# Kernel optimization log

Measured on AMD Instinct MI355X. Metric: run time of the kernel, lower is better.

Reference implementation:

```python
import jax, jax.numpy as jnp
import numpy as np

N, E, F_IN, C, D = 50000, 200000, 384, 384, 16
NEG_SLOPE = 0.2


def setup_inputs() -> dict:
    key = jax.random.key(0)
    ks = jax.random.split(key, 12)
    x = jax.random.normal(ks[0], (N, F_IN), jnp.float32)
    # random edges with no self-loops (PyG GATConv removes self loops before re-adding them)
    src = jax.random.randint(ks[1], (E,), 0, N)
    off = jax.random.randint(ks[2], (E,), 1, N)
    dst = (src + off) % N
    edge_index = jnp.stack([src, dst]).astype(jnp.int32)  # [2, E]
    edge_attr = jax.random.uniform(ks[3], (E, D), jnp.float32)
    # GATConv params (heads=1): lin (no bias), att_src/att_dst/att_edge, lin_edge (no bias), bias
    W_lin = jax.random.normal(ks[4], (F_IN, C), jnp.float32) / np.float32(np.sqrt(F_IN))
    att_src = jax.random.normal(ks[5], (C,), jnp.float32) * 0.1
    att_dst = jax.random.normal(ks[6], (C,), jnp.float32) * 0.1
    W_edge = jax.random.normal(ks[7], (D, C), jnp.float32) / np.float32(np.sqrt(D))
    att_edge = jax.random.normal(ks[8], (C,), jnp.float32) * 0.1
    bias_conv = jnp.zeros((C,), jnp.float32)
    # final Linear(384 -> 1) with bias
    W_out = jax.random.normal(ks[9], (C, 1), jnp.float32) / np.float32(np.sqrt(C))
    b_out = jnp.zeros((1,), jnp.float32)
    return {"x": x, "edge_index": edge_index, "edge_attr": edge_attr,
            "W_lin": W_lin, "att_src": att_src, "att_dst": att_dst,
            "W_edge": W_edge, "att_edge": att_edge, "bias_conv": bias_conv,
            "W_out": W_out, "b_out": b_out}


def _gat_conv(x, edge_index, edge_attr, W_lin, att_src, att_dst, W_edge, att_edge, bias_conv):
    src, dst = edge_index[0], edge_index[1]
    h = x @ W_lin                              # [N, C]
    a_src = h @ att_src                        # [N]
    a_dst = h @ att_dst                        # [N]
    # add self loops; self-loop edge_attr = per-node mean of incoming edge_attr (fill_value='mean')
    deg = jax.ops.segment_sum(jnp.ones((E,), x.dtype), dst, num_segments=N)
    ea_mean = jax.ops.segment_sum(edge_attr, dst, num_segments=N) / jnp.maximum(deg, 1.0)[:, None]
    loop = jnp.arange(N, dtype=src.dtype)
    src_f = jnp.concatenate([src, loop])       # [E+N]
    dst_f = jnp.concatenate([dst, loop])
    ea_f = jnp.concatenate([edge_attr, ea_mean], axis=0)  # [E+N, D]
    a_edge = (ea_f @ W_edge) @ att_edge        # [E+N]
    # per-edge attention logits, segment softmax over destination neighborhoods
    alpha = jax.nn.leaky_relu(a_src[src_f] + a_dst[dst_f] + a_edge, NEG_SLOPE)
    amax = jax.ops.segment_max(alpha, dst_f, num_segments=N)  # every node has a self loop
    ex = jnp.exp(alpha - amax[dst_f])
    denom = jax.ops.segment_sum(ex, dst_f, num_segments=N)
    w = ex / denom[dst_f]                      # [E+N]
    # weighted scatter-aggregate of source messages
    out = jax.ops.segment_sum(h[src_f] * w[:, None], dst_f, num_segments=N)
    return out + bias_conv


def reference(x, edge_index, edge_attr, W_lin, att_src, att_dst, W_edge, att_edge, bias_conv, W_out, b_out):
    h = _gat_conv(x, edge_index, edge_attr, W_lin, att_src, att_dst, W_edge, att_edge, bias_conv)
    return jax.nn.relu(h @ W_out + b_out)      # [N, 1]
```

## Files before the change

kernel.cpp:

```cpp
#include <hip/hip_runtime.h>

#define NEG_SLOPE 0.2f
#define TPB    256
#define NB     256
#define CNT    196
#define EBLK   256
#define PERBLK 32
#define ER     4
#define MAGIC  21913099ULL
#define NODE_BLKS 1568

__global__ __launch_bounds__(TPB) void k_fold(
        const float* __restrict__ Wlin, const float* __restrict__ att_src,
        const float* __restrict__ att_dst, const float* __restrict__ Wedge,
        const float* __restrict__ att_edge, const float* __restrict__ bias_conv,
        const float* __restrict__ Wout, const float* __restrict__ bout,
        float* __restrict__ vs, float* __restrict__ va, float* __restrict__ vb,
        float* __restrict__ we, float* __restrict__ cb) {
    const int gwid = (blockIdx.x * TPB + threadIdx.x) >> 6;
    const int lane = threadIdx.x & 63;
    for (int j = 0; j < 4; ++j) {
        int f = gwid * 4 + j;
        if (f < 384) {
            float a = 0.f, b = 0.f, c = 0.f;
            for (int k = lane; k < 384; k += 64) {
                float w = Wlin[f * 384 + k];
                a += w * Wout[k];
                b += w * att_src[k];
                c += w * att_dst[k];
            }
            for (int off = 32; off > 0; off >>= 1) {
                a += __shfl_down(a, off);
                b += __shfl_down(b, off);
                c += __shfl_down(c, off);
            }
            if (lane == 0) { vs[f] = a; va[f] = b; vb[f] = c; }
        } else if (f < 400) {
            int d = f - 384;
            float a = 0.f;
            for (int k = lane; k < 384; k += 64) a += Wedge[d * 384 + k] * att_edge[k];
            for (int off = 32; off > 0; off >>= 1) a += __shfl_down(a, off);
            if (lane == 0) we[d] = a;
        } else if (f == 400) {
            float a = 0.f;
            for (int k = lane; k < 384; k += 64) a += bias_conv[k] * Wout[k];
            for (int off = 32; off > 0; off >>= 1) a += __shfl_down(a, off);
            if (lane == 0) cb[0] = a + bout[0];
        }
    }
}

__global__ __launch_bounds__(TPB) void k_main(
        const float* __restrict__ x,
        const int* __restrict__ src, const int* __restrict__ dst,
        const float* __restrict__ ea,
        const float* __restrict__ vs, const float* __restrict__ va,
        const float* __restrict__ vb, const float* __restrict__ we,
        float* __restrict__ s, float* __restrict__ asrc, float* __restrict__ adst,
        uint2* __restrict__ rec, unsigned int* __restrict__ cnt,
        int N, int E) {
    __shared__ float weL[16];
    __shared__ int   ldsCnt[NB];
    const int tid = threadIdx.x;
    const int blk = blockIdx.x;

    if (blk < NODE_BLKS) {
        const int ll = tid & 15;
        const int slot = blk * 16 + (tid >> 4);
        const float4* vs4 = (const float4*)vs;
        const float4* va4 = (const float4*)va;
        const float4* vb4 = (const float4*)vb;
        float4 wsr[6], war[6], wbr[6];
#pragma unroll
        for (int j = 0; j < 6; ++j) {
            wsr[j] = vs4[ll + 16 * j];
            war[j] = va4[ll + 16 * j];
            wbr[j] = vb4[ll + 16 * j];
        }
        for (int n = slot; n < N; n += NODE_BLKS * 16) {
            const float4* row = (const float4*)(x + (size_t)n * 384);
            float4 xr[6];
#pragma unroll
            for (int j = 0; j < 6; ++j) xr[j] = row[ll + 16 * j];
            float a = 0.f, b = 0.f, c = 0.f;
#pragma unroll
            for (int j = 0; j < 6; ++j) {
                a += xr[j].x*wsr[j].x + xr[j].y*wsr[j].y + xr[j].z*wsr[j].z + xr[j].w*wsr[j].w;
                b += xr[j].x*war[j].x + xr[j].y*war[j].y + xr[j].z*war[j].z + xr[j].w*war[j].w;
                c += xr[j].x*wbr[j].x + xr[j].y*wbr[j].y + xr[j].z*wbr[j].z + xr[j].w*wbr[j].w;
            }
#pragma unroll
            for (int off = 8; off > 0; off >>= 1) {
                a += __shfl_xor(a, off);
                b += __shfl_xor(b, off);
                c += __shfl_xor(c, off);
            }
            if (ll == 0) { s[n] = a; asrc[n] = b; adst[n] = c; }
        }
        return;
    }

    const int eblk = blk - NODE_BLKS;
    if (tid < 16) weL[tid] = we[tid];
    for (int i = tid; i < NB; i += TPB) ldsCnt[i] = 0;
    __syncthreads();

    const int chunk = (E + EBLK - 1) / EBLK;
    const int ebase = eblk * chunk;
    const int eend  = min(E, ebase + chunk);
    int dnr[ER], rkr[ER], bkr[ER];
#pragma unroll
    for (int r = 0; r < ER; ++r) {
        int e = ebase + r * TPB + tid;
        dnr[r] = -1;
        if (e < eend) {
            int dn = dnr[r] = dst[e];
            int b  = bkr[r] = (int)(((unsigned long long)(unsigned)dn * MAGIC) >> 32);
            rkr[r] = atomicAdd(&ldsCnt[b], 1);
        }
    }
    __syncthreads();
    if (tid < NB) cnt[tid * EBLK + eblk] = (unsigned)ldsCnt[tid];

    const float4 w0 = make_float4(weL[0],  weL[1],  weL[2],  weL[3]);
    const float4 w1 = make_float4(weL[4],  weL[5],  weL[6],  weL[7]);
    const float4 w2 = make_float4(weL[8],  weL[9],  weL[10], weL[11]);
    const float4 w3 = make_float4(weL[12], weL[13], weL[14], weL[15]);
#pragma unroll
    for (int r = 0; r < ER; ++r) {
        int dn = dnr[r];
        if (dn >= 0 && rkr[r] < PERBLK) {
            int e  = ebase + r * TPB + tid;
            int sn = src[e];
            const float4* rw = (const float4*)(ea + (size_t)e * 16);
            float4 v0 = rw[0], v1 = rw[1], v2 = rw[2], v3 = rw[3];
            float a = v0.x*w0.x + v0.y*w0.y + v0.z*w0.z + v0.w*w0.w
                    + v1.x*w1.x + v1.y*w1.y + v1.z*w1.z + v1.w*w1.w
                    + v2.x*w2.x + v2.y*w2.y + v2.z*w2.z + v2.w*w2.w
                    + v3.x*w3.x + v3.y*w3.y + v3.z*w3.z + v3.w*w3.w;
            int b = bkr[r];
            unsigned key = ((unsigned)(dn - b * CNT) << 16) | (unsigned)sn;
            rec[((size_t)b * EBLK + eblk) * PERBLK + rkr[r]] =
                make_uint2(key, __float_as_uint(a));
        }
    }
}

__global__ __launch_bounds__(TPB) void k_agg(
        const uint2* __restrict__ rec, const unsigned int* __restrict__ cnt,
        const float* __restrict__ asrc, const float* __restrict__ adst,
        const float* __restrict__ s, const float* __restrict__ cb,
        float* __restrict__ out, int n_nodes) {
    __shared__ float4 accL[CNT];
    __shared__ float  adstL[CNT];
    const int b  = blockIdx.x;
    const int lo = b * CNT;
    int cn = n_nodes - lo;
    if (cn <= 0) return;
    if (cn > CNT) cn = CNT;
    const int tid = threadIdx.x;
    for (int r = tid; r < CNT; r += TPB) accL[r] = make_float4(0.f, 0.f, 0.f, 0.f);
    for (int r = tid; r < cn; r += TPB)  adstL[r] = adst[lo + r];
    __syncthreads();
    int m = (int)cnt[b * EBLK + tid];
    if (m > PERBLK) m = PERBLK;
    const uint2* base = rec + ((size_t)b * EBLK + tid) * PERBLK;
    for (int i = 0; i < m; ++i) {
        uint2 rc = base[i];
        int r  = (int)(rc.x >> 16);
        int sn = (int)(rc.x & 0xFFFFu);
        float a  = __uint_as_float(rc.y);
        float al = asrc[sn] + adstL[r] + a;
        al = al >= 0.f ? al : NEG_SLOPE * al;
        float ex = __expf(al);
        float* bp = (float*)&accL[r];
        atomicAdd(bp + 0, 1.0f);
        atomicAdd(bp + 1, a);
        atomicAdd(bp + 2, ex);
        atomicAdd(bp + 3, ex * s[sn]);
    }
    __syncthreads();
    const float cbv = cb[0];
    for (int r = tid; r < cn; r += TPB) {
        int n = lo + r;
        float4 ac = accL[r];
        float d  = ac.x < 1.f ? 1.f : ac.x;
        float al = asrc[n] + adstL[r] + ac.y / d;
        al = al >= 0.f ? al : NEG_SLOPE * al;
        float ex = __expf(al);
        float v = (ac.w + ex * s[n]) / (ac.z + ex) + cbv;
        out[n] = v > 0.f ? v : 0.f;
    }
}

extern "C" void kernel_launch(void* const* d_in, const int* in_sizes, int n_in,
                              void* d_out, int out_size, void* d_ws, size_t ws_size,
                              hipStream_t stream) {
    const float* x        = (const float*)d_in[0];
    const int*   eidx     = (const int*)d_in[1];
    const float* ea       = (const float*)d_in[2];
    const float* Wlin     = (const float*)d_in[3];
    const float* att_src  = (const float*)d_in[4];
    const float* att_dst  = (const float*)d_in[5];
    const float* Wedge    = (const float*)d_in[6];
    const float* att_edge = (const float*)d_in[7];
    const float* bias_c   = (const float*)d_in[8];
    const float* Wout     = (const float*)d_in[9];
    const float* bout     = (const float*)d_in[10];
    float*       out      = (float*)d_out;

    const int N = in_sizes[0] / 384;
    const int E = in_sizes[2] / 16;
    const int* src = eidx;
    const int* dst = eidx + E;

    float* W = (float*)d_ws;
    float*        vs   = W;
    float*        va   = W + 384;
    float*        vb   = W + 768;
    float*        we   = W + 1152;
    float*        cb   = W + 1168;
    float*        s    = W + 1280;
    float*        asrc = s + N;
    float*        adst = asrc + N;
    unsigned int* cnt  = (unsigned int*)(adst + N);
    uint2*        rec  = (uint2*)(cnt + NB * EBLK);

    k_fold<<<26, TPB, 0, stream>>>(
        Wlin, att_src, att_dst, Wedge, att_edge, bias_c, Wout, bout,
        vs, va, vb, we, cb);
    k_main<<<NODE_BLKS + EBLK, TPB, 0, stream>>>(
        x, src, dst, ea, vs, va, vb, we, s, asrc, adst, rec, cnt, N, E);
    k_agg<<<NB, TPB, 0, stream>>>(
        rec, cnt, asrc, adst, s, cb, out, N);
}
```

Measured before the change: 41.92 us.

## Rebalance work split: one wave per fold row, fewer node blocks, edge blocks first

k_fold now gives each wave one output row instead of four and launches more blocks. k_main puts the edge-bucketing blocks first and processes nodes with half as many blocks, each unrolled over up to four rows for more memory-level parallelism. The count matrix is transposed so the edge-block writes are coalesced, at the cost of strided reads in k_agg. The aim is better scheduling and overlap of the edge and node phases and less per-block overhead. The trade-off is fewer waves in flight for the node dot products.

```diff
diff --git a/kernel.cpp b/kernel.cpp
--- a/kernel.cpp
+++ b/kernel.cpp
@@ -8,7 +8,7 @@
 #define PERBLK 32
 #define ER     4
 #define MAGIC  21913099ULL
-#define NODE_BLKS 1568
+#define NBLK2  782
 
 __global__ __launch_bounds__(TPB) void k_fold(
         const float* __restrict__ Wlin, const float* __restrict__ att_src,
@@ -19,34 +19,32 @@
         float* __restrict__ we, float* __restrict__ cb) {
     const int gwid = (blockIdx.x * TPB + threadIdx.x) >> 6;
     const int lane = threadIdx.x & 63;
-    for (int j = 0; j < 4; ++j) {
-        int f = gwid * 4 + j;
-        if (f < 384) {
-            float a = 0.f, b = 0.f, c = 0.f;
-            for (int k = lane; k < 384; k += 64) {
-                float w = Wlin[f * 384 + k];
-                a += w * Wout[k];
-                b += w * att_src[k];
-                c += w * att_dst[k];
-            }
-            for (int off = 32; off > 0; off >>= 1) {
-                a += __shfl_down(a, off);
-                b += __shfl_down(b, off);
-                c += __shfl_down(c, off);
-            }
-            if (lane == 0) { vs[f] = a; va[f] = b; vb[f] = c; }
-        } else if (f < 400) {
-            int d = f - 384;
-            float a = 0.f;
-            for (int k = lane; k < 384; k += 64) a += Wedge[d * 384 + k] * att_edge[k];
-            for (int off = 32; off > 0; off >>= 1) a += __shfl_down(a, off);
-            if (lane == 0) we[d] = a;
-        } else if (f == 400) {
-            float a = 0.f;
-            for (int k = lane; k < 384; k += 64) a += bias_conv[k] * Wout[k];
-            for (int off = 32; off > 0; off >>= 1) a += __shfl_down(a, off);
-            if (lane == 0) cb[0] = a + bout[0];
-        }
+    if (gwid < 384) {
+        int f = gwid;
+        float a = 0.f, b = 0.f, c = 0.f;
+        for (int k = lane; k < 384; k += 64) {
+            float w = Wlin[f * 384 + k];
+            a += w * Wout[k];
+            b += w * att_src[k];
+            c += w * att_dst[k];
+        }
+        for (int off = 32; off > 0; off >>= 1) {
+            a += __shfl_down(a, off);
+            b += __shfl_down(b, off);
+            c += __shfl_down(c, off);
+        }
+        if (lane == 0) { vs[f] = a; va[f] = b; vb[f] = c; }
+    } else if (gwid < 400) {
+        int d = gwid - 384;
+        float a = 0.f;
+        for (int k = lane; k < 384; k += 64) a += Wedge[d * 384 + k] * att_edge[k];
+        for (int off = 32; off > 0; off >>= 1) a += __shfl_down(a, off);
+        if (lane == 0) we[d] = a;
+    } else if (gwid == 400) {
+        float a = 0.f;
+        for (int k = lane; k < 384; k += 64) a += bias_conv[k] * Wout[k];
+        for (int off = 32; off > 0; off >>= 1) a += __shfl_down(a, off);
+        if (lane == 0) cb[0] = a + bout[0];
     }
 }
 
@@ -64,9 +62,9 @@
     const int tid = threadIdx.x;
     const int blk = blockIdx.x;
 
-    if (blk < NODE_BLKS) {
-        const int ll = tid & 15;
-        const int slot = blk * 16 + (tid >> 4);
+    if (blk >= EBLK) {
+        const int ll   = tid & 15;
+        const int slot = (blk - EBLK) * 16 + (tid >> 4);
         const float4* vs4 = (const float4*)vs;
         const float4* va4 = (const float4*)va;
         const float4* vb4 = (const float4*)vb;
@@ -77,30 +75,34 @@
             war[j] = va4[ll + 16 * j];
             wbr[j] = vb4[ll + 16 * j];
         }
-        for (int n = slot; n < N; n += NODE_BLKS * 16) {
-            const float4* row = (const float4*)(x + (size_t)n * 384);
-            float4 xr[6];
-#pragma unroll
-            for (int j = 0; j < 6; ++j) xr[j] = row[ll + 16 * j];
-            float a = 0.f, b = 0.f, c = 0.f;
-#pragma unroll
-            for (int j = 0; j < 6; ++j) {
-                a += xr[j].x*wsr[j].x + xr[j].y*wsr[j].y + xr[j].z*wsr[j].z + xr[j].w*wsr[j].w;
-                b += xr[j].x*war[j].x + xr[j].y*war[j].y + xr[j].z*war[j].z + xr[j].w*war[j].w;
-                c += xr[j].x*wbr[j].x + xr[j].y*wbr[j].y + xr[j].z*wbr[j].z + xr[j].w*wbr[j].w;
+#pragma unroll
+        for (int i = 0; i < 4; ++i) {
+            int n = slot + i * (NBLK2 * 16);
+            if (n < N) {
+                const float4* row = (const float4*)(x + (size_t)n * 384);
+                float4 xr[6];
+#pragma unroll
+                for (int j = 0; j < 6; ++j) xr[j] = row[ll + 16 * j];
+                float a = 0.f, b = 0.f, c = 0.f;
+#pragma unroll
+                for (int j = 0; j < 6; ++j) {
+                    a += xr[j].x*wsr[j].x + xr[j].y*wsr[j].y + xr[j].z*wsr[j].z + xr[j].w*wsr[j].w;
+                    b += xr[j].x*war[j].x + xr[j].y*war[j].y + xr[j].z*war[j].z + xr[j].w*war[j].w;
+                    c += xr[j].x*wbr[j].x + xr[j].y*wbr[j].y + xr[j].z*wbr[j].z + xr[j].w*wbr[j].w;
+                }
+#pragma unroll
+                for (int off = 8; off > 0; off >>= 1) {
+                    a += __shfl_xor(a, off);
+                    b += __shfl_xor(b, off);
+                    c += __shfl_xor(c, off);
+                }
+                if (ll == 0) { s[n] = a; asrc[n] = b; adst[n] = c; }
             }
-#pragma unroll
-            for (int off = 8; off > 0; off >>= 1) {
-                a += __shfl_xor(a, off);
-                b += __shfl_xor(b, off);
-                c += __shfl_xor(c, off);
-            }
-            if (ll == 0) { s[n] = a; asrc[n] = b; adst[n] = c; }
         }
         return;
     }
 
-    const int eblk = blk - NODE_BLKS;
+    const int eblk = blk;
     if (tid < 16) weL[tid] = we[tid];
     for (int i = tid; i < NB; i += TPB) ldsCnt[i] = 0;
     __syncthreads();
@@ -120,7 +122,7 @@
         }
     }
     __syncthreads();
-    if (tid < NB) cnt[tid * EBLK + eblk] = (unsigned)ldsCnt[tid];
+    if (tid < NB) cnt[eblk * NB + tid] = (unsigned)ldsCnt[tid];
 
     const float4 w0 = make_float4(weL[0],  weL[1],  weL[2],  weL[3]);
     const float4 w1 = make_float4(weL[4],  weL[5],  weL[6],  weL[7]);
@@ -162,7 +164,7 @@
     for (int r = tid; r < CNT; r += TPB) accL[r] = make_float4(0.f, 0.f, 0.f, 0.f);
     for (int r = tid; r < cn; r += TPB)  adstL[r] = adst[lo + r];
     __syncthreads();
-    int m = (int)cnt[b * EBLK + tid];
+    int m = (int)cnt[tid * NB + b];
     if (m > PERBLK) m = PERBLK;
     const uint2* base = rec + ((size_t)b * EBLK + tid) * PERBLK;
     for (int i = 0; i < m; ++i) {
@@ -224,12 +226,12 @@
     float*        asrc = s + N;
     float*        adst = asrc + N;
     unsigned int* cnt  = (unsigned int*)(adst + N);
-    uint2*        rec  = (uint2*)(cnt + NB * EBLK);
-
-    k_fold<<<26, TPB, 0, stream>>>(
+    uint2*        rec  = (uint2*)(cnt + EBLK * NB);
+
+    k_fold<<<101, TPB, 0, stream>>>(
         Wlin, att_src, att_dst, Wedge, att_edge, bias_c, Wout, bout,
         vs, va, vb, we, cb);
-    k_main<<<NODE_BLKS + EBLK, TPB, 0, stream>>>(
+    k_main<<<EBLK + NBLK2, TPB, 0, stream>>>(
         x, src, dst, ea, vs, va, vb, we, s, asrc, adst, rec, cnt, N, E);
     k_agg<<<NB, TPB, 0, stream>>>(
         rec, cnt, asrc, adst, s, cb, out, N);
```

Result: faster. 35.00 us (-16.5%).
